# Performance work log

Measured on AMD Instinct MI355X. Metric: run time of the kernel, lower is better.

## Reference

```python
import jax, jax.numpy as jnp
import numpy as np

L, B, D, H, DM = 4, 32768, 64, 256, 32
NS = 8            # fixed RK4 steps standing in for adaptive Dormand-Prince (atol=1e-5)
EPS = 1e-3        # keras BatchNormalization epsilon


def setup_inputs() -> dict:
    key = jax.random.key(0)
    ks = jax.random.split(key, 16)
    g = lambda k, shape, s=0.05: jax.random.normal(k, shape, jnp.float32) * s
    perm = jnp.concatenate([jnp.arange(DM, D), jnp.arange(DM)]).astype(jnp.int32)
    return {
        'x': jax.random.normal(ks[0], (B, D), jnp.float32),
        'perms': jnp.tile(perm[None, :], (L, 1)),
        'nvp_W0': g(ks[1], (L, DM, H)), 'nvp_b0': jnp.zeros((L, H), jnp.float32),
        'nvp_W1': g(ks[2], (L, H, H)), 'nvp_b1': jnp.zeros((L, H), jnp.float32),
        'nvp_W2': g(ks[3], (L, H, 2 * (D - DM))), 'nvp_b2': jnp.zeros((L, 2 * (D - DM)), jnp.float32),
        'ode_W0': g(ks[4], (L, D + 1, H)), 'ode_b0': jnp.zeros((L, H), jnp.float32),
        'ode_W1': g(ks[5], (L, H, H)), 'ode_b1': jnp.zeros((L, H), jnp.float32),
        'ode_W2': g(ks[6], (L, H, D)), 'ode_b2': jnp.zeros((L, D), jnp.float32),
        'bn1_mean': g(ks[7], (L, D), 0.1), 'bn1_var': jax.random.uniform(ks[8], (L, D), jnp.float32, 0.5, 1.5),
        'bn1_gamma': jax.random.uniform(ks[9], (L, D), jnp.float32, 0.8, 1.2), 'bn1_beta': g(ks[10], (L, D), 0.1),
        'bn2_mean': g(ks[11], (L, D), 0.1), 'bn2_var': jax.random.uniform(ks[12], (L, D), jnp.float32, 0.5, 1.5),
        'bn2_gamma': jax.random.uniform(ks[13], (L, D), jnp.float32, 0.8, 1.2), 'bn2_beta': g(ks[14], (L, D), 0.1),
    }


def _nvp(x, W0, b0, W1, b1, W2, b2):
    # RealNVP coupling: pass-through masked half, affine-transform the rest
    x0, x1 = x[:, :DM], x[:, DM:]
    h = jax.nn.relu(x0 @ W0 + b0)
    h = jax.nn.relu(h @ W1 + b1)
    shift, log_scale = jnp.split(h @ W2 + b2, 2, axis=-1)
    return jnp.concatenate([x0, x1 * jnp.exp(log_scale) + shift], axis=-1)


def _bn_fwd(x, mean, var, gamma, beta):
    # TFP BatchNormalization bijector forward == de-normalization
    return (x - beta) * jnp.sqrt(var + EPS) / gamma + mean


def _ffjord(x, W0, b0, W1, b1, W2, b2):
    # integrate dx/dt = MLP([t, x]) from t=0 to t=1 (fixed-step RK4)
    def f(t, y):
        ty = jnp.concatenate([jnp.full((y.shape[0], 1), t, y.dtype), y], axis=-1)
        h = jnp.tanh(ty @ W0 + b0)
        h = jnp.tanh(h @ W1 + b1)
        return h @ W2 + b2

    dt = 1.0 / NS

    def step(y, t):
        k1 = f(t, y)
        k2 = f(t + dt / 2, y + (dt / 2) * k1)
        k3 = f(t + dt / 2, y + (dt / 2) * k2)
        k4 = f(t + dt, y + dt * k3)
        return y + (dt / 6) * (k1 + 2 * k2 + 2 * k3 + k4), None

    ts = jnp.arange(NS, dtype=x.dtype) * dt
    y, _ = jax.lax.scan(step, x, ts)
    return y


def reference(x, perms, nvp_W0, nvp_b0, nvp_W1, nvp_b1, nvp_W2, nvp_b2,
              ode_W0, ode_b0, ode_W1, ode_b1, ode_W2, ode_b2,
              bn1_mean, bn1_var, bn1_gamma, bn1_beta,
              bn2_mean, bn2_var, bn2_gamma, bn2_beta):
    for i in range(L):  # per layer: Permute -> RealNVP -> BN -> FFJORD -> BN
        x = x[:, perms[i]]
        x = _nvp(x, nvp_W0[i], nvp_b0[i], nvp_W1[i], nvp_b1[i], nvp_W2[i], nvp_b2[i])
        x = _bn_fwd(x, bn1_mean[i], bn1_var[i], bn1_gamma[i], bn1_beta[i])
        x = _ffjord(x, ode_W0[i], ode_b0[i], ode_W1[i], ode_b1[i], ode_W2[i], ode_b2[i])
        x = _bn_fwd(x, bn2_mean[i], bn2_var[i], bn2_gamma[i], bn2_beta[i])
    return x
```

## Files before the change

### kernel.cpp

```cpp
#include <hip/hip_runtime.h>
#include <hip/hip_bf16.h>


#define LNUM   4
#define NSTEP  8
#define EPSV   1e-3f

typedef __attribute__((ext_vector_type(8))) short  short8;
typedef __attribute__((ext_vector_type(4))) float  floatx4;

#define MF(a, b, c) __builtin_amdgcn_mfma_f32_16x16x32_bf16((a), (b), (c), 0, 0, 0)

#define OW0_OFF 0
#define OW1_OFF 65536
#define OW2_OFF 327680
#define NW0_OFF 393216
#define NW1_OFF 425984
#define NW2_OFF 688128
#define WS_ELEMS 753664

#define W1B_OFF  0
#define H1_OFF   81920
#define H2_OFF   114688
#define YIN_OFF  147456
#define PARS_OFF 155648
#define LDS_SIZE 158976

__device__ __forceinline__ unsigned short f2bfu_rne(float f) {
  unsigned int u = __float_as_uint(f);
  return (unsigned short)((u + 0x7FFFu + ((u >> 16) & 1u)) >> 16);
}

__device__ __forceinline__ unsigned long long pack4bf(float a, float b, float c, float d) {
  __hip_bfloat162 lo = __float22bfloat162_rn(make_float2(a, b));
  __hip_bfloat162 hi = __float22bfloat162_rn(make_float2(c, d));
  unsigned int ul, uh;
  __builtin_memcpy(&ul, &lo, 4);
  __builtin_memcpy(&uh, &hi, 4);
  return (unsigned long long)ul | ((unsigned long long)uh << 32);
}

__device__ __forceinline__ float bfu2f(unsigned short u) {
  return __uint_as_float((unsigned int)u << 16);
}

__device__ __forceinline__ float tanh_fast2(float v) {
  float e = __expf(v);
  return 1.0f - 2.0f * __builtin_amdgcn_rcpf(e + 1.0f);
}

__global__ void prep_kernel(const float* __restrict__ odeW0, const float* __restrict__ odeW1,
                            const float* __restrict__ odeW2, const float* __restrict__ nvpW0,
                            const float* __restrict__ nvpW1, const float* __restrict__ nvpW2,
                            unsigned short* __restrict__ ws) {
  int idx = blockIdx.x * blockDim.x + threadIdx.x;
  if (idx >= WS_ELEMS) return;
  const float* W; int base, K, N, lstride, skip; float scale;
  int f = idx;
  if (f < OW1_OFF)      { W = odeW0; base = OW0_OFF; K = 64;  N = 256; lstride = 16640; skip = 1; scale = 2.f; f -= OW0_OFF; }
  else if (f < OW2_OFF) { W = odeW1; base = OW1_OFF; K = 256; N = 256; lstride = 65536; skip = 0; scale = 2.f; f -= OW1_OFF; }
  else if (f < NW0_OFF) { W = odeW2; base = OW2_OFF; K = 256; N = 64;  lstride = 16384; skip = 0; scale = 1.f; f -= OW2_OFF; }
  else if (f < NW1_OFF) { W = nvpW0; base = NW0_OFF; K = 32;  N = 256; lstride = 8192;  skip = 0; scale = 1.f; f -= NW0_OFF; }
  else if (f < NW2_OFF) { W = nvpW1; base = NW1_OFF; K = 256; N = 256; lstride = 65536; skip = 0; scale = 1.f; f -= NW1_OFF; }
  else                  { W = nvpW2; base = NW2_OFF; K = 256; N = 64;  lstride = 16384; skip = 0; scale = 1.f; f -= NW2_OFF; }
  int per   = K * N;
  int layer = f / per;
  int e     = f - layer * per;
  int j  = e & 7;
  int l  = (e >> 3) & 63;
  int t  = e >> 9;
  int KS = K >> 5; if (KS < 1) KS = 1;
  int ks = t % KS;
  int nt = t / KS;
  int n = nt * 16 + (l & 15);
  int k = ks * 32 + ((l >> 4) << 3) + j;
  ws[base + layer * per + e] = f2bfu_rne(scale * W[layer * lstride + (k + skip) * N + n]);
}

__device__ __forceinline__ void st_h(char* dst, int m, int n0, float a, float b, float c, float d) {
  int off = (m * 512 + n0 * 2) ^ ((m & 15) << 4);
  *reinterpret_cast<unsigned long long*>(dst + off) = pack4bf(a, b, c, d);
}

__global__ void
__launch_bounds__(512)
flow_kernel(const float* __restrict__ xin,
            const float* __restrict__ nvp_b0, const float* __restrict__ nvp_b1,
            const float* __restrict__ nvp_b2,
            const float* __restrict__ odeW0_full,
            const float* __restrict__ ode_b0, const float* __restrict__ ode_b1,
            const float* __restrict__ ode_b2,
            const float* __restrict__ bn1m, const float* __restrict__ bn1v,
            const float* __restrict__ bn1g, const float* __restrict__ bn1b,
            const float* __restrict__ bn2m, const float* __restrict__ bn2v,
            const float* __restrict__ bn2g, const float* __restrict__ bn2b,
            const unsigned short* __restrict__ ws,
            float* __restrict__ out) {
  __shared__ __align__(16) char smem[LDS_SIZE];
  short8* w1b = reinterpret_cast<short8*>(smem + W1B_OFF);
  char*  h1   = smem + H1_OFF;
  char*  h2   = smem + H2_OFF;
  char*  yinb = smem + YIN_OFF;
  char*  shfb = smem + H1_OFF;
  float* pars = reinterpret_cast<float*>(smem + PARS_OFF);

  const floatx4 zero4 = {0.f, 0.f, 0.f, 0.f};

  const int tid  = threadIdx.x;
  const int lane = tid & 63;
  const int w    = tid >> 6;
  const int l15  = lane & 15;
  const int g    = lane >> 4;
  const int wn   = w & 3;
  const int wm   = w >> 2;
  const int nb   = w * 32;
  const int row0 = blockIdx.x * 64;
  const int d0   = wn * 16 + g * 4;
  const float dtv = 1.0f / NSTEP;

  float y[8];
  #pragma unroll
  for (int mt = 0; mt < 2; ++mt) {
    int m = wm * 32 + mt * 16 + l15;
    floatx4 v = *reinterpret_cast<const floatx4*>(xin + (row0 + m) * 64 + d0);
    y[mt * 4 + 0] = v[0]; y[mt * 4 + 1] = v[1]; y[mt * 4 + 2] = v[2]; y[mt * 4 + 3] = v[3];
  }

  short8 aw0[2][2];
  short8 aw1h[2][3];
  short8 aw2[8];

  for (int l = 0; l < LNUM; ++l) {
    __syncthreads();
    {
      const short8* src = reinterpret_cast<const short8*>(ws + NW1_OFF + l * 65536);
      #pragma unroll 2
      for (int i = tid; i < 5120; i += 512) {
        int ks3 = i >> 10;
        int rem = i & 1023;
        w1b[i] = src[((rem >> 6) << 9) + ((3 + ks3) << 6) + (rem & 63)];
      }
    }
    #pragma unroll
    for (int mt = 0; mt < 2; ++mt) {
      int m = wm * 32 + mt * 16 + l15;
      if (wn >= 2) {
        int off = (m * 128 + (d0 - 32) * 2) ^ ((m & 7) << 4);
        *reinterpret_cast<unsigned long long*>(yinb + off) =
            pack4bf(y[mt * 4 + 0], y[mt * 4 + 1], y[mt * 4 + 2], y[mt * 4 + 3]);
      } else {
        int off = (m * 128 + 64 + d0 * 2) ^ ((m & 7) << 4);
        *reinterpret_cast<unsigned long long*>(yinb + off) =
            pack4bf(y[mt * 4 + 0], y[mt * 4 + 1], y[mt * 4 + 2], y[mt * 4 + 3]);
      }
    }
    for (int i = tid; i < 576; i += 512) {
      float v;
      if (i < 256)      v = nvp_b0[l * 256 + i];
      else if (i < 512) v = nvp_b1[l * 256 + i - 256];
      else              v = nvp_b2[l * 64 + i - 512];
      pars[i] = v;
    }
    {
      const short8* p0 = reinterpret_cast<const short8*>(ws + NW0_OFF + l * 8192);
      const short8* p1 = reinterpret_cast<const short8*>(ws + NW1_OFF + l * 65536);
      const short8* p2 = reinterpret_cast<const short8*>(ws + NW2_OFF + l * 16384);
      aw0[0][0] = p0[(w * 2 + 0) * 64 + lane];
      aw0[1][0] = p0[(w * 2 + 1) * 64 + lane];
      #pragma unroll
      for (int nt = 0; nt < 2; ++nt)
        #pragma unroll
        for (int ks = 0; ks < 3; ++ks) aw1h[nt][ks] = p1[((w * 2 + nt) * 8 + ks) * 64 + lane];
      #pragma unroll
      for (int ks = 0; ks < 8; ++ks) aw2[ks] = p2[(wn * 8 + ks) * 64 + lane];
    }
    __syncthreads();

    #pragma unroll
    for (int mh = 0; mh < 2; ++mh) {
      floatx4 acc[2][2];
      #pragma unroll
      for (int nt = 0; nt < 2; ++nt)
        #pragma unroll
        for (int mt = 0; mt < 2; ++mt) acc[nt][mt] = zero4;
      short8 B[2];
      #pragma unroll
      for (int mt = 0; mt < 2; ++mt) {
        int m = mh * 32 + mt * 16 + l15;
        int off = (m * 128 + g * 16) ^ ((m & 7) << 4);
        B[mt] = *reinterpret_cast<const short8*>(yinb + off);
      }
      #pragma unroll
      for (int nt = 0; nt < 2; ++nt)
        #pragma unroll
        for (int mt = 0; mt < 2; ++mt) acc[nt][mt] = MF(aw0[nt][0], B[mt], acc[nt][mt]);
      #pragma unroll
      for (int nt = 0; nt < 2; ++nt) {
        int nbase = nb + nt * 16 + g * 4;
        floatx4 bb = *reinterpret_cast<const floatx4*>(pars + nbase);
        #pragma unroll
        for (int mt = 0; mt < 2; ++mt) {
          int m = mh * 32 + mt * 16 + l15;
          st_h(h1, m, nbase,
               fmaxf(acc[nt][mt][0] + bb[0], 0.f), fmaxf(acc[nt][mt][1] + bb[1], 0.f),
               fmaxf(acc[nt][mt][2] + bb[2], 0.f), fmaxf(acc[nt][mt][3] + bb[3], 0.f));
        }
      }
    }
    __syncthreads();

    #pragma unroll
    for (int mh = 0; mh < 2; ++mh) {
      floatx4 acc[2][2];
      #pragma unroll
      for (int nt = 0; nt < 2; ++nt)
        #pragma unroll
        for (int mt = 0; mt < 2; ++mt) acc[nt][mt] = zero4;
      #pragma unroll
      for (int ks = 0; ks < 8; ++ks) {
        short8 A[2], B[2];
        if (ks < 3) {
          A[0] = aw1h[0][ks]; A[1] = aw1h[1][ks];
        } else {
          A[0] = w1b[((ks - 3) << 10) + (w * 2 + 0) * 64 + lane];
          A[1] = w1b[((ks - 3) << 10) + (w * 2 + 1) * 64 + lane];
        }
        #pragma unroll
        for (int mt = 0; mt < 2; ++mt) {
          int m = mh * 32 + mt * 16 + l15;
          int off = (m * 512 + (ks * 32 + g * 8) * 2) ^ ((m & 15) << 4);
          B[mt] = *reinterpret_cast<const short8*>(h1 + off);
        }
        #pragma unroll
        for (int nt = 0; nt < 2; ++nt)
          #pragma unroll
          for (int mt = 0; mt < 2; ++mt) acc[nt][mt] = MF(A[nt], B[mt], acc[nt][mt]);
      }
      #pragma unroll
      for (int nt = 0; nt < 2; ++nt) {
        int nbase = nb + nt * 16 + g * 4;
        floatx4 bb = *reinterpret_cast<const floatx4*>(pars + 256 + nbase);
        #pragma unroll
        for (int mt = 0; mt < 2; ++mt) {
          int m = mh * 32 + mt * 16 + l15;
          st_h(h2, m, nbase,
               fmaxf(acc[nt][mt][0] + bb[0], 0.f), fmaxf(acc[nt][mt][1] + bb[1], 0.f),
               fmaxf(acc[nt][mt][2] + bb[2], 0.f), fmaxf(acc[nt][mt][3] + bb[3], 0.f));
        }
      }
    }
    __syncthreads();

    floatx4 a3[2];
    a3[0] = zero4; a3[1] = zero4;
    #pragma unroll
    for (int ks = 0; ks < 8; ++ks) {
      #pragma unroll
      for (int mt = 0; mt < 2; ++mt) {
        int m = wm * 32 + mt * 16 + l15;
        int off = (m * 512 + (ks * 32 + g * 8) * 2) ^ ((m & 15) << 4);
        short8 B = *reinterpret_cast<const short8*>(h2 + off);
        a3[mt] = MF(aw2[ks], B, a3[mt]);
      }
    }
    {
      floatx4 b2v = *reinterpret_cast<const floatx4*>(pars + 512 + d0);
      #pragma unroll
      for (int mt = 0; mt < 2; ++mt)
        #pragma unroll
        for (int p = 0; p < 4; ++p) a3[mt][p] += b2v[p];
    }

    {
      const short8* src = reinterpret_cast<const short8*>(ws + OW1_OFF + l * 65536);
      #pragma unroll 2
      for (int i = tid; i < 5120; i += 512) {
        int ks3 = i >> 10;
        int rem = i & 1023;
        w1b[i] = src[((rem >> 6) << 9) + ((3 + ks3) << 6) + (rem & 63)];
      }
    }
    if (wn < 2) {
      #pragma unroll
      for (int mt = 0; mt < 2; ++mt) {
        int m = wm * 32 + mt * 16 + l15;
        int off = (m * 64 + d0 * 2) ^ ((m & 3) << 4);
        *reinterpret_cast<unsigned long long*>(shfb + off) =
            pack4bf(a3[mt][0], a3[mt][1], a3[mt][2], a3[mt][3]);
      }
    }
    __syncthreads();

    #pragma unroll
    for (int mt = 0; mt < 2; ++mt) {
      int m = wm * 32 + mt * 16 + l15;
      if (wn < 2) {
        int off = (m * 128 + d0 * 2) ^ ((m & 7) << 4);
        unsigned long long u = *reinterpret_cast<const unsigned long long*>(yinb + off);
        y[mt * 4 + 0] = bfu2f((unsigned short)(u));
        y[mt * 4 + 1] = bfu2f((unsigned short)(u >> 16));
        y[mt * 4 + 2] = bfu2f((unsigned short)(u >> 32));
        y[mt * 4 + 3] = bfu2f((unsigned short)(u >> 48));
      } else {
        int offx = (m * 128 + 64 + (d0 - 32) * 2) ^ ((m & 7) << 4);
        unsigned long long ux = *reinterpret_cast<const unsigned long long*>(yinb + offx);
        int offs = (m * 64 + (d0 - 32) * 2) ^ ((m & 3) << 4);
        unsigned long long us = *reinterpret_cast<const unsigned long long*>(shfb + offs);
        y[mt * 4 + 0] = bfu2f((unsigned short)(ux)) * __expf(a3[mt][0]) + bfu2f((unsigned short)(us));
        y[mt * 4 + 1] = bfu2f((unsigned short)(ux >> 16)) * __expf(a3[mt][1]) + bfu2f((unsigned short)(us >> 16));
        y[mt * 4 + 2] = bfu2f((unsigned short)(ux >> 32)) * __expf(a3[mt][2]) + bfu2f((unsigned short)(us >> 32));
        y[mt * 4 + 3] = bfu2f((unsigned short)(ux >> 48)) * __expf(a3[mt][3]) + bfu2f((unsigned short)(us >> 48));
      }
    }
    {
      floatx4 mm = *reinterpret_cast<const floatx4*>(bn1m + l * 64 + d0);
      floatx4 vv = *reinterpret_cast<const floatx4*>(bn1v + l * 64 + d0);
      floatx4 gg = *reinterpret_cast<const floatx4*>(bn1g + l * 64 + d0);
      floatx4 be = *reinterpret_cast<const floatx4*>(bn1b + l * 64 + d0);
      float sc[4];
      #pragma unroll
      for (int p = 0; p < 4; ++p) sc[p] = sqrtf(vv[p] + EPSV) / gg[p];
      #pragma unroll
      for (int mt = 0; mt < 2; ++mt)
        #pragma unroll
        for (int p = 0; p < 4; ++p)
          y[mt * 4 + p] = (y[mt * 4 + p] - be[p]) * sc[p] + mm[p];
    }

    for (int i = tid; i < 832; i += 512) {
      float v;
      if (i < 256)      v = 2.f * ode_b0[l * 256 + i];
      else if (i < 512) v = 2.f * ode_b1[l * 256 + i - 256];
      else if (i < 576) v = ode_b2[l * 64 + i - 512];
      else              v = 2.f * odeW0_full[l * 16640 + i - 576];
      pars[i] = v;
    }
    {
      const short8* p0 = reinterpret_cast<const short8*>(ws + OW0_OFF + l * 16384);
      const short8* p1 = reinterpret_cast<const short8*>(ws + OW1_OFF + l * 65536);
      const short8* p2 = reinterpret_cast<const short8*>(ws + OW2_OFF + l * 16384);
      #pragma unroll
      for (int nt = 0; nt < 2; ++nt)
        #pragma unroll
        for (int ks = 0; ks < 2; ++ks) aw0[nt][ks] = p0[((w * 2 + nt) * 2 + ks) * 64 + lane];
      #pragma unroll
      for (int nt = 0; nt < 2; ++nt)
        #pragma unroll
        for (int ks = 0; ks < 3; ++ks) aw1h[nt][ks] = p1[((w * 2 + nt) * 8 + ks) * 64 + lane];
      #pragma unroll
      for (int ks = 0; ks < 8; ++ks) aw2[ks] = p2[(wn * 8 + ks) * 64 + lane];
    }
    __syncthreads();

    float ka[8], kc[8];
    for (int s = 0; s < NSTEP; ++s) {
      float t0 = (float)s * dtv;
      for (int stg = 0; stg < 4; ++stg) {
        float cadd = (stg == 0) ? 0.0f : ((stg == 3) ? dtv : 0.5f * dtv);
        float tcur = t0 + cadd;
        #pragma unroll
        for (int mt = 0; mt < 2; ++mt) {
          int m = wm * 32 + mt * 16 + l15;
          float v0, v1, v2, v3;
          if (stg == 0) {
            v0 = y[mt * 4 + 0]; v1 = y[mt * 4 + 1]; v2 = y[mt * 4 + 2]; v3 = y[mt * 4 + 3];
          } else {
            v0 = fmaf(cadd, kc[mt * 4 + 0], y[mt * 4 + 0]);
            v1 = fmaf(cadd, kc[mt * 4 + 1], y[mt * 4 + 1]);
            v2 = fmaf(cadd, kc[mt * 4 + 2], y[mt * 4 + 2]);
            v3 = fmaf(cadd, kc[mt * 4 + 3], y[mt * 4 + 3]);
          }
          int off = (m * 128 + d0 * 2) ^ ((m & 7) << 4);
          *reinterpret_cast<unsigned long long*>(yinb + off) = pack4bf(v0, v1, v2, v3);
        }
        __syncthreads();

        #pragma unroll
        for (int mh = 0; mh < 2; ++mh) {
          floatx4 acc[2][2];
          #pragma unroll
          for (int nt = 0; nt < 2; ++nt)
            #pragma unroll
            for (int mt = 0; mt < 2; ++mt) acc[nt][mt] = zero4;
          #pragma unroll
          for (int ks = 0; ks < 2; ++ks) {
            short8 B[2];
            #pragma unroll
            for (int mt = 0; mt < 2; ++mt) {
              int m = mh * 32 + mt * 16 + l15;
              int off = (m * 128 + (ks * 32 + g * 8) * 2) ^ ((m & 7) << 4);
              B[mt] = *reinterpret_cast<const short8*>(yinb + off);
            }
            #pragma unroll
            for (int nt = 0; nt < 2; ++nt)
              #pragma unroll
              for (int mt = 0; mt < 2; ++mt) acc[nt][mt] = MF(aw0[nt][ks], B[mt], acc[nt][mt]);
          }
          #pragma unroll
          for (int nt = 0; nt < 2; ++nt) {
            int nbase = nb + nt * 16 + g * 4;
            floatx4 bb = *reinterpret_cast<const floatx4*>(pars + nbase);
            floatx4 w0 = *reinterpret_cast<const floatx4*>(pars + 576 + nbase);
            float c0 = bb[0] + tcur * w0[0], c1 = bb[1] + tcur * w0[1];
            float c2 = bb[2] + tcur * w0[2], c3 = bb[3] + tcur * w0[3];
            #pragma unroll
            for (int mt = 0; mt < 2; ++mt) {
              int m = mh * 32 + mt * 16 + l15;
              st_h(h1, m, nbase,
                   tanh_fast2(acc[nt][mt][0] + c0), tanh_fast2(acc[nt][mt][1] + c1),
                   tanh_fast2(acc[nt][mt][2] + c2), tanh_fast2(acc[nt][mt][3] + c3));
            }
          }
        }
        __syncthreads();

        #pragma unroll
        for (int mh = 0; mh < 2; ++mh) {
          floatx4 acc[2][2];
          #pragma unroll
          for (int nt = 0; nt < 2; ++nt)
            #pragma unroll
            for (int mt = 0; mt < 2; ++mt) acc[nt][mt] = zero4;
          #pragma unroll
          for (int ks = 0; ks < 8; ++ks) {
            short8 A[2], B[2];
            if (ks < 3) {
              A[0] = aw1h[0][ks]; A[1] = aw1h[1][ks];
            } else {
              A[0] = w1b[((ks - 3) << 10) + (w * 2 + 0) * 64 + lane];
              A[1] = w1b[((ks - 3) << 10) + (w * 2 + 1) * 64 + lane];
            }
            #pragma unroll
            for (int mt = 0; mt < 2; ++mt) {
              int m = mh * 32 + mt * 16 + l15;
              int off = (m * 512 + (ks * 32 + g * 8) * 2) ^ ((m & 15) << 4);
              B[mt] = *reinterpret_cast<const short8*>(h1 + off);
            }
            #pragma unroll
            for (int nt = 0; nt < 2; ++nt)
              #pragma unroll
              for (int mt = 0; mt < 2; ++mt) acc[nt][mt] = MF(A[nt], B[mt], acc[nt][mt]);
          }
          #pragma unroll
          for (int nt = 0; nt < 2; ++nt) {
            int nbase = nb + nt * 16 + g * 4;
            floatx4 bb = *reinterpret_cast<const floatx4*>(pars + 256 + nbase);
            #pragma unroll
            for (int mt = 0; mt < 2; ++mt) {
              int m = mh * 32 + mt * 16 + l15;
              st_h(h2, m, nbase,
                   tanh_fast2(acc[nt][mt][0] + bb[0]), tanh_fast2(acc[nt][mt][1] + bb[1]),
                   tanh_fast2(acc[nt][mt][2] + bb[2]), tanh_fast2(acc[nt][mt][3] + bb[3]));
            }
          }
        }
        __syncthreads();

        {
          floatx4 a2[2];
          a2[0] = zero4; a2[1] = zero4;
          #pragma unroll
          for (int ks = 0; ks < 8; ++ks) {
            #pragma unroll
            for (int mt = 0; mt < 2; ++mt) {
              int m = wm * 32 + mt * 16 + l15;
              int off = (m * 512 + (ks * 32 + g * 8) * 2) ^ ((m & 15) << 4);
              short8 B = *reinterpret_cast<const short8*>(h2 + off);
              a2[mt] = MF(aw2[ks], B, a2[mt]);
            }
          }
          floatx4 b2v = *reinterpret_cast<const floatx4*>(pars + 512 + d0);
          #pragma unroll
          for (int mt = 0; mt < 2; ++mt)
            #pragma unroll
            for (int p = 0; p < 4; ++p)
              kc[mt * 4 + p] = a2[mt][p] + b2v[p];
        }
        if (stg == 0) {
          #pragma unroll
          for (int i = 0; i < 8; ++i) ka[i] = kc[i];
        } else if (stg == 3) {
          #pragma unroll
          for (int i = 0; i < 8; ++i) ka[i] += kc[i];
        } else {
          #pragma unroll
          for (int i = 0; i < 8; ++i) ka[i] += 2.0f * kc[i];
        }
      }
      #pragma unroll
      for (int i = 0; i < 8; ++i) y[i] += (dtv / 6.0f) * ka[i];
    }

    {
      floatx4 mm = *reinterpret_cast<const floatx4*>(bn2m + l * 64 + d0);
      floatx4 vv = *reinterpret_cast<const floatx4*>(bn2v + l * 64 + d0);
      floatx4 gg = *reinterpret_cast<const floatx4*>(bn2g + l * 64 + d0);
      floatx4 be = *reinterpret_cast<const floatx4*>(bn2b + l * 64 + d0);
      float sc[4];
      #pragma unroll
      for (int p = 0; p < 4; ++p) sc[p] = sqrtf(vv[p] + EPSV) / gg[p];
      #pragma unroll
      for (int mt = 0; mt < 2; ++mt)
        #pragma unroll
        for (int p = 0; p < 4; ++p)
          y[mt * 4 + p] = (y[mt * 4 + p] - be[p]) * sc[p] + mm[p];
    }
  }

  #pragma unroll
  for (int mt = 0; mt < 2; ++mt) {
    int m = wm * 32 + mt * 16 + l15;
    floatx4 v = {y[mt * 4 + 0], y[mt * 4 + 1], y[mt * 4 + 2], y[mt * 4 + 3]};
    *reinterpret_cast<floatx4*>(out + (row0 + m) * 64 + d0) = v;
  }
}

extern "C" void kernel_launch(void* const* d_in, const int* in_sizes, int n_in,
                              void* d_out, int out_size, void* d_ws, size_t ws_size,
                              hipStream_t stream) {
  const float* x      = (const float*)d_in[0];
  const float* nvpW0  = (const float*)d_in[2];
  const float* nvp_b0 = (const float*)d_in[3];
  const float* nvpW1  = (const float*)d_in[4];
  const float* nvp_b1 = (const float*)d_in[5];
  const float* nvpW2  = (const float*)d_in[6];
  const float* nvp_b2 = (const float*)d_in[7];
  const float* odeW0  = (const float*)d_in[8];
  const float* ode_b0 = (const float*)d_in[9];
  const float* odeW1  = (const float*)d_in[10];
  const float* ode_b1 = (const float*)d_in[11];
  const float* odeW2  = (const float*)d_in[12];
  const float* ode_b2 = (const float*)d_in[13];
  const float* bn1m   = (const float*)d_in[14];
  const float* bn1v   = (const float*)d_in[15];
  const float* bn1g   = (const float*)d_in[16];
  const float* bn1b   = (const float*)d_in[17];
  const float* bn2m   = (const float*)d_in[18];
  const float* bn2v   = (const float*)d_in[19];
  const float* bn2g   = (const float*)d_in[20];
  const float* bn2b   = (const float*)d_in[21];
  unsigned short* ws  = (unsigned short*)d_ws;
  float* out          = (float*)d_out;

  int pblocks = (WS_ELEMS + 255) / 256;
  prep_kernel<<<pblocks, 256, 0, stream>>>(odeW0, odeW1, odeW2, nvpW0, nvpW1, nvpW2, ws);
  flow_kernel<<<512, 512, 0, stream>>>(x, nvp_b0, nvp_b1, nvp_b2, odeW0,
                                       ode_b0, ode_b1, ode_b2,
                                       bn1m, bn1v, bn1g, bn1b,
                                       bn2m, bn2v, bn2g, bn2b,
                                       ws, out);
}
```

Measured before the change: 1.253 ms.

## Stream W1 hidden weights from global/L2 instead of staging in LDS

Removes the 80KB LDS staging buffer for the 256x256 W1 matrices. Register-held slices drop from 3 to 2 k-steps, and the remaining 6 k-steps are read directly from global memory inside the inner MFMA loops. LDS use falls from about 159KB to about 77KB, which could allow two blocks per CU and removes the per-layer copy into LDS. The cost is repeated global/L2 loads of the weights on every RK4 stage, which adds load latency to the critical GEMM loop.

```diff
diff --git a/kernel.cpp b/kernel.cpp
--- a/kernel.cpp
+++ b/kernel.cpp
@@ -19,12 +19,11 @@
 #define NW2_OFF 688128
 #define WS_ELEMS 753664
 
-#define W1B_OFF  0
-#define H1_OFF   81920
-#define H2_OFF   114688
-#define YIN_OFF  147456
-#define PARS_OFF 155648
-#define LDS_SIZE 158976
+#define H1_OFF   0
+#define H2_OFF   32768
+#define YIN_OFF  65536
+#define PARS_OFF 73728
+#define LDS_SIZE 77056
 
 __device__ __forceinline__ unsigned short f2bfu_rne(float f) {
   unsigned int u = __float_as_uint(f);
@@ -97,7 +96,6 @@
             const unsigned short* __restrict__ ws,
             float* __restrict__ out) {
   __shared__ __align__(16) char smem[LDS_SIZE];
-  short8* w1b = reinterpret_cast<short8*>(smem + W1B_OFF);
   char*  h1   = smem + H1_OFF;
   char*  h2   = smem + H2_OFF;
   char*  yinb = smem + YIN_OFF;
@@ -127,20 +125,14 @@
   }
 
   short8 aw0[2][2];
-  short8 aw1h[2][3];
+  short8 aw1h[2][2];
   short8 aw2[8];
 
   for (int l = 0; l < LNUM; ++l) {
+    const short8* w1nvp = reinterpret_cast<const short8*>(ws + NW1_OFF + l * 65536);
+    const short8* w1ode = reinterpret_cast<const short8*>(ws + OW1_OFF + l * 65536);
+
     __syncthreads();
-    {
-      const short8* src = reinterpret_cast<const short8*>(ws + NW1_OFF + l * 65536);
-      #pragma unroll 2
-      for (int i = tid; i < 5120; i += 512) {
-        int ks3 = i >> 10;
-        int rem = i & 1023;
-        w1b[i] = src[((rem >> 6) << 9) + ((3 + ks3) << 6) + (rem & 63)];
-      }
-    }
     #pragma unroll
     for (int mt = 0; mt < 2; ++mt) {
       int m = wm * 32 + mt * 16 + l15;
@@ -163,14 +155,13 @@
     }
     {
       const short8* p0 = reinterpret_cast<const short8*>(ws + NW0_OFF + l * 8192);
-      const short8* p1 = reinterpret_cast<const short8*>(ws + NW1_OFF + l * 65536);
       const short8* p2 = reinterpret_cast<const short8*>(ws + NW2_OFF + l * 16384);
       aw0[0][0] = p0[(w * 2 + 0) * 64 + lane];
       aw0[1][0] = p0[(w * 2 + 1) * 64 + lane];
       #pragma unroll
       for (int nt = 0; nt < 2; ++nt)
         #pragma unroll
-        for (int ks = 0; ks < 3; ++ks) aw1h[nt][ks] = p1[((w * 2 + nt) * 8 + ks) * 64 + lane];
+        for (int ks = 0; ks < 2; ++ks) aw1h[nt][ks] = w1nvp[((w * 2 + nt) * 8 + ks) * 64 + lane];
       #pragma unroll
       for (int ks = 0; ks < 8; ++ks) aw2[ks] = p2[(wn * 8 + ks) * 64 + lane];
     }
@@ -219,11 +210,11 @@
       #pragma unroll
       for (int ks = 0; ks < 8; ++ks) {
         short8 A[2], B[2];
-        if (ks < 3) {
+        if (ks < 2) {
           A[0] = aw1h[0][ks]; A[1] = aw1h[1][ks];
         } else {
-          A[0] = w1b[((ks - 3) << 10) + (w * 2 + 0) * 64 + lane];
-          A[1] = w1b[((ks - 3) << 10) + (w * 2 + 1) * 64 + lane];
+          A[0] = w1nvp[((w * 2 + 0) * 8 + ks) * 64 + lane];
+          A[1] = w1nvp[((w * 2 + 1) * 8 + ks) * 64 + lane];
         }
         #pragma unroll
         for (int mt = 0; mt < 2; ++mt) {
@@ -271,15 +262,6 @@
         for (int p = 0; p < 4; ++p) a3[mt][p] += b2v[p];
     }
 
-    {
-      const short8* src = reinterpret_cast<const short8*>(ws + OW1_OFF + l * 65536);
-      #pragma unroll 2
-      for (int i = tid; i < 5120; i += 512) {
-        int ks3 = i >> 10;
-        int rem = i & 1023;
-        w1b[i] = src[((rem >> 6) << 9) + ((3 + ks3) << 6) + (rem & 63)];
-      }
-    }
     if (wn < 2) {
       #pragma unroll
       for (int mt = 0; mt < 2; ++mt) {
@@ -337,7 +319,6 @@
     }
     {
       const short8* p0 = reinterpret_cast<const short8*>(ws + OW0_OFF + l * 16384);
-      const short8* p1 = reinterpret_cast<const short8*>(ws + OW1_OFF + l * 65536);
       const short8* p2 = reinterpret_cast<const short8*>(ws + OW2_OFF + l * 16384);
       #pragma unroll
       for (int nt = 0; nt < 2; ++nt)
@@ -346,7 +327,7 @@
       #pragma unroll
       for (int nt = 0; nt < 2; ++nt)
         #pragma unroll
-        for (int ks = 0; ks < 3; ++ks) aw1h[nt][ks] = p1[((w * 2 + nt) * 8 + ks) * 64 + lane];
+        for (int ks = 0; ks < 2; ++ks) aw1h[nt][ks] = w1ode[((w * 2 + nt) * 8 + ks) * 64 + lane];
       #pragma unroll
       for (int ks = 0; ks < 8; ++ks) aw2[ks] = p2[(wn * 8 + ks) * 64 + lane];
     }
@@ -424,11 +405,11 @@
           #pragma unroll
           for (int ks = 0; ks < 8; ++ks) {
             short8 A[2], B[2];
-            if (ks < 3) {
+            if (ks < 2) {
               A[0] = aw1h[0][ks]; A[1] = aw1h[1][ks];
             } else {
-              A[0] = w1b[((ks - 3) << 10) + (w * 2 + 0) * 64 + lane];
-              A[1] = w1b[((ks - 3) << 10) + (w * 2 + 1) * 64 + lane];
+              A[0] = w1ode[((w * 2 + 0) * 8 + ks) * 64 + lane];
+              A[1] = w1ode[((w * 2 + 1) * 8 + ks) * 64 + lane];
             }
             #pragma unroll
             for (int mt = 0; mt < 2; ++mt) {
```

Result: no change. 1.249 ms (-0.3%).
